# Kernel optimization log

Hardware: AMD Instinct MI355X
Metric: run time of the kernel (lower is better)

Reference implementation:

```python
import jax, jax.numpy as jnp
import numpy as np

GRID_SIZE = 3
SPLINE_ORDER = 3

def make_grid():
    # grid_range=[-1,1], h=2/grid_size; extended grid of length grid_size+2k+1 = 10
    h = 2.0 / GRID_SIZE
    return (jnp.arange(-SPLINE_ORDER, GRID_SIZE + SPLINE_ORDER + 1, dtype=jnp.float32) * h - 1.0)

def b_splines(x, grid):
    # x: [N, F] -> bases [N, F, grid_size+spline_order]
    xg = x[..., None]
    bases = ((xg >= grid[:-1]) & (xg < grid[1:])).astype(x.dtype)
    for j in range(1, SPLINE_ORDER + 1):
        left = (xg - grid[: -(j + 1)]) / (grid[j:-1] - grid[: -(j + 1)])
        right = (grid[j + 1:] - xg) / (grid[j + 1:] - grid[1:-j])
        bases = left * bases[..., :-1] + right * bases[..., 1:]
    return bases

def kan_linear(x, base_w, spline_w, scaler, grid):
    # x: [N, F]; base_w: [O, F]; spline_w: [O, F, G]; scaler: [O, F]
    base = jax.nn.silu(x) @ base_w.T
    sb = b_splines(x, grid)                      # [N, F, G]
    spl = jnp.einsum('nfg,ofg->no', sb, spline_w * scaler[..., None])
    return base + spl

def kan_conv3x3(x, base_w, spline_w, scaler, grid):
    # x: [B, C, H, W]; 3x3 kernel, pad 1, stride 1 -> [B, O, H, W]
    B, C, H, W = x.shape
    patches = jax.lax.conv_general_dilated_patches(
        x, (3, 3), (1, 1), ((1, 1), (1, 1)))     # [B, C*9, H, W]
    p = patches.transpose(0, 2, 3, 1).reshape(B * H * W, C * 9)
    y = kan_linear(p, base_w, spline_w, scaler, grid)
    return y.reshape(B, H, W, -1).transpose(0, 3, 1, 2)

def maxpool2(x):
    return jax.lax.reduce_window(x, -jnp.inf, jax.lax.max,
                                 (1, 1, 2, 2), (1, 1, 2, 2), 'VALID')

def setup_inputs() -> dict:
    key = jax.random.key(0)
    ks = jax.random.split(key, 12)
    s = 0.1
    return {
        'x': jax.random.normal(ks[0], (256, 3, 32, 32), jnp.float32),
        'c1_base_w': jax.random.normal(ks[1], (8, 27), jnp.float32) * s,
        'c1_spline_w': jax.random.normal(ks[2], (8, 27, 6), jnp.float32) * s,
        'c1_scaler': jax.random.normal(ks[3], (8, 27), jnp.float32) * s,
        'c2_base_w': jax.random.normal(ks[4], (16, 72), jnp.float32) * s,
        'c2_spline_w': jax.random.normal(ks[5], (16, 72, 6), jnp.float32) * s,
        'c2_scaler': jax.random.normal(ks[6], (16, 72), jnp.float32) * s,
        'c3_base_w': jax.random.normal(ks[7], (32, 144), jnp.float32) * s,
        'c3_spline_w': jax.random.normal(ks[8], (32, 144, 6), jnp.float32) * s,
        'c3_scaler': jax.random.normal(ks[9], (32, 144), jnp.float32) * s,
        'lin_w': jax.random.normal(ks[10], (100, 512), jnp.float32) * s,
        'lin_b': jax.random.normal(ks[11], (100,), jnp.float32) * s,
    }

def reference(x, c1_base_w, c1_spline_w, c1_scaler,
              c2_base_w, c2_spline_w, c2_scaler,
              c3_base_w, c3_spline_w, c3_scaler,
              lin_w, lin_b):
    grid = make_grid()
    h = maxpool2(kan_conv3x3(x, c1_base_w, c1_spline_w, c1_scaler, grid))   # [B,8,16,16]
    h = maxpool2(kan_conv3x3(h, c2_base_w, c2_spline_w, c2_scaler, grid))   # [B,16,8,8]
    h = maxpool2(kan_conv3x3(h, c3_base_w, c3_spline_w, c3_scaler, grid))   # [B,32,4,4]
    h = h.reshape(h.shape[0], -1)                                           # [B,512]
    return h @ lin_w.T + lin_b                                              # [B,100]
```

## Files before the change

kernel.cpp:

```cpp
#include <hip/hip_runtime.h>
#include <math.h>


#define BATCH 256

typedef short bf16x8 __attribute__((ext_vector_type(8)));
typedef float f32x4  __attribute__((ext_vector_type(4)));

__device__ __forceinline__ unsigned f2bf(float f) {
    unsigned u = __float_as_uint(f);
    u += 0x7fffu + ((u >> 16) & 1u);
    return u >> 16;
}
__device__ __forceinline__ unsigned pk2(float a, float b) {
    return f2bf(a) | (f2bf(b) << 16);
}

__device__ __forceinline__ void bspline_basis(float x, float bs[6]) {
    const float h = 2.0f / 3.0f;
    float g[10];
#pragma unroll
    for (int i = 0; i < 10; ++i) g[i] = (float)(i - 3) * h - 1.0f;
    float b[9];
#pragma unroll
    for (int i = 0; i < 9; ++i) b[i] = (x >= g[i] && x < g[i + 1]) ? 1.0f : 0.0f;
#pragma unroll
    for (int j = 1; j <= 3; ++j) {
        const float inv_d = 1.0f / ((float)j * h);
#pragma unroll
        for (int i = 0; i + j < 9; ++i) {
            float left  = (x - g[i]) * inv_d;
            float right = (g[i + j + 1] - x) * inv_d;
            b[i] = left * b[i] + right * b[i + 1];
        }
    }
#pragma unroll
    for (int i = 0; i < 6; ++i) bs[i] = b[i];
}

__device__ __forceinline__ uint4 act_record(float val) {
    float silu = val / (1.0f + __expf(-val));
    float bs[6];
    bspline_basis(val, bs);
    uint4 r;
    r.x = pk2(silu, bs[0]);
    r.y = pk2(bs[1], bs[2]);
    r.z = pk2(bs[3], bs[4]);
    r.w = f2bf(bs[5]);
    return r;
}

__device__ __forceinline__ uint4 fuse_w(const float* bw, const float* sw,
                                        const float* sc, int j) {
    float s = sc[j];
    uint4 r;
    r.x = pk2(bw[j],             sw[j * 6 + 0] * s);
    r.y = pk2(sw[j * 6 + 1] * s, sw[j * 6 + 2] * s);
    r.z = pk2(sw[j * 6 + 3] * s, sw[j * 6 + 4] * s);
    r.w = f2bf(sw[j * 6 + 5] * s);
    return r;
}

__global__ __launch_bounds__(512, 4) void kan_l1(
        const float* __restrict__ x,
        const float* __restrict__ bw, const float* __restrict__ sw,
        const float* __restrict__ sc,
        const float* __restrict__ bw3, const float* __restrict__ sw3,
        const float* __restrict__ sc3,
        uint4* __restrict__ w3g,
        float* __restrict__ out) {
    constexpr int C = 3, H = 32, W = 32, F = 27, FP = 28, NS = 7;
    constexpr int RT = 18, TC = 34, NT = 512;

    __shared__ uint4 s_act[C * RT * TC];
    __shared__ uint4 s_w[FP * 16];

    const int tid = threadIdx.x;
    const int bid = blockIdx.x;
    const int b   = bid >> 1;
    const int v   = bid & 1;

    if (bid < 9) {
        int i = bid * NT + tid;
        if (i < 4608) {
            int o = i / 144, fp = i % 144;
            w3g[fp * 32 + o] = fuse_w(bw3, sw3, sc3, i);
        }
    }

    for (int i = tid; i < FP * 16; i += NT) {
        int fp = i >> 4, o = i & 15;
        uint4 r = make_uint4(0u, 0u, 0u, 0u);
        if (fp < F && o < 8) r = fuse_w(bw, sw, sc, o * F + fp);
        s_w[i] = r;
    }

    const int r0 = 16 * v - 1;
    const float* xb = x + (size_t)b * C * H * W;
    for (int i = tid; i < C * RT * TC; i += NT) {
        int cc  = i / (RT * TC);
        int rr  = (i / TC) % RT;
        int col = i % TC;
        int gr = r0 + rr, gc = col - 1;
        float val = 0.0f;
        if ((unsigned)gr < (unsigned)H && (unsigned)gc < (unsigned)W)
            val = xb[(cc * H + gr) * W + gc];
        s_act[i] = act_record(val);
    }
    __syncthreads();

    const int lane = tid & 63;
    const int wv   = tid >> 6;
    const int kg   = lane >> 4;
    const int oc   = lane & 15;
    const int m    = lane & 15;

    bf16x8 bfr[NS];
#pragma unroll
    for (int s = 0; s < NS; ++s)
        bfr[s] = *reinterpret_cast<const bf16x8*>(&s_w[(4 * s + kg) * 16 + oc]);

    int pixoff[4];
#pragma unroll
    for (int t = 0; t < 4; ++t)
        pixoff[t] = (2 * wv + (t >> 1)) * TC + 16 * (t & 1) + m;

    f32x4 acc[4];
#pragma unroll
    for (int t = 0; t < 4; ++t) acc[t] = (f32x4){0.f, 0.f, 0.f, 0.f};

#pragma unroll
    for (int s = 0; s < NS; ++s) {
        int tp = 4 * s + kg;
        tp = (tp > F - 1) ? F - 1 : tp;
        int c  = tp / 9;
        int t9 = tp - 9 * c;
        int ky = t9 / 3;
        int kx = t9 - 3 * ky;
        int base = (c * RT + ky) * TC + kx;
#pragma unroll
        for (int t = 0; t < 4; ++t) {
            bf16x8 a = *reinterpret_cast<const bf16x8*>(&s_act[base + pixoff[t]]);
            acc[t] = __builtin_amdgcn_mfma_f32_16x16x32_bf16(a, bfr[s], acc[t], 0, 0, 0);
        }
    }

    if (oc < 8) {
        f32x4 e0, e1;
#pragma unroll
        for (int p = 0; p < 4; ++p) {
            e0[p] = fmaxf(acc[0][p], acc[2][p]);
            e1[p] = fmaxf(acc[1][p], acc[3][p]);
        }
        float* op = out + (((size_t)b * 8 + oc) * 16 + (8 * v + wv)) * 16;
        op[2 * kg]         = fmaxf(e0[0], e0[1]);
        op[2 * kg + 1]     = fmaxf(e0[2], e0[3]);
        op[8 + 2 * kg]     = fmaxf(e1[0], e1[1]);
        op[8 + 2 * kg + 1] = fmaxf(e1[2], e1[3]);
    }
}

__global__ __launch_bounds__(512, 2) void kan_l2l3lin(
        const float* __restrict__ h1,
        const float* __restrict__ bw2, const float* __restrict__ sw2,
        const float* __restrict__ sc2,
        const uint4* __restrict__ w3g,
        const float* __restrict__ lin_w, const float* __restrict__ lin_b,
        float* __restrict__ out) {
    constexpr int NT = 512;
    __shared__ alignas(16) unsigned char s_mem[59904];
    uint4* s_act2 = (uint4*)s_mem;
    uint4* s_w2   = (uint4*)(s_mem + 41472);
    float* s_h2   = (float*)s_mem;
    uint4* s_act3 = (uint4*)(s_mem + 4096);
    float* s_h3   = (float*)s_mem;

    const int tid = threadIdx.x;
    const int n   = blockIdx.x;
    const int lane = tid & 63;
    const int wv   = tid >> 6;
    const int kg   = lane >> 4;
    const int oc   = lane & 15;
    const int m    = lane & 15;

    for (int i = tid; i < 72 * 16; i += NT) {
        int fp = i >> 4, o = i & 15;
        s_w2[i] = fuse_w(bw2, sw2, sc2, o * 72 + fp);
    }
    const float* xb = h1 + (size_t)n * 8 * 16 * 16;
    for (int i = tid; i < 8 * 18 * 18; i += NT) {
        int cc  = i / 324;
        int rr  = (i / 18) % 18;
        int col = i % 18;
        int gr = rr - 1, gc = col - 1;
        float val = 0.0f;
        if ((unsigned)gr < 16u && (unsigned)gc < 16u)
            val = xb[(cc * 16 + gr) * 16 + gc];
        s_act2[i] = act_record(val);
    }
    __syncthreads();

    {
        bf16x8 bfr2[18];
#pragma unroll
        for (int s = 0; s < 18; ++s)
            bfr2[s] = *reinterpret_cast<const bf16x8*>(&s_w2[(4 * s + kg) * 16 + oc]);
        const int p0 = (2 * wv) * 18 + m;
        const int p1 = (2 * wv + 1) * 18 + m;
        f32x4 a0 = (f32x4){0.f, 0.f, 0.f, 0.f};
        f32x4 a1 = (f32x4){0.f, 0.f, 0.f, 0.f};
#pragma unroll
        for (int s = 0; s < 18; ++s) {
            int tp = 4 * s + kg;
            int c  = tp / 9;
            int t9 = tp - 9 * c;
            int ky = t9 / 3;
            int kx = t9 - 3 * ky;
            int base = (c * 18 + ky) * 18 + kx;
            bf16x8 av0 = *reinterpret_cast<const bf16x8*>(&s_act2[base + p0]);
            a0 = __builtin_amdgcn_mfma_f32_16x16x32_bf16(av0, bfr2[s], a0, 0, 0, 0);
            bf16x8 av1 = *reinterpret_cast<const bf16x8*>(&s_act2[base + p1]);
            a1 = __builtin_amdgcn_mfma_f32_16x16x32_bf16(av1, bfr2[s], a1, 0, 0, 0);
        }
        float e0 = fmaxf(a0[0], a1[0]);
        float e1 = fmaxf(a0[1], a1[1]);
        float e2 = fmaxf(a0[2], a1[2]);
        float e3 = fmaxf(a0[3], a1[3]);
        __syncthreads();
        s_h2[(oc * 8 + wv) * 8 + 2 * kg]     = fmaxf(e0, e1);
        s_h2[(oc * 8 + wv) * 8 + 2 * kg + 1] = fmaxf(e2, e3);
    }
    __syncthreads();

    for (int i = tid; i < 16 * 10 * 10; i += NT) {
        int cc  = i / 100;
        int rr  = (i / 10) % 10;
        int col = i % 10;
        int gr = rr - 1, gc = col - 1;
        float val = 0.0f;
        if ((unsigned)gr < 8u && (unsigned)gc < 8u)
            val = s_h2[(cc * 8 + gr) * 8 + gc];
        s_act3[i] = act_record(val);
    }
    __syncthreads();

    {
        const int mt  = wv & 3;
        const int o03 = 16 * (wv >> 2);
        bf16x8 bfr3[36];
#pragma unroll
        for (int s = 0; s < 36; ++s)
            bfr3[s] = *reinterpret_cast<const bf16x8*>(&w3g[(4 * s + kg) * 32 + o03 + oc]);
        const int poff = (2 * mt + (m >> 3)) * 10 + (m & 7);
        f32x4 a3 = (f32x4){0.f, 0.f, 0.f, 0.f};
#pragma unroll
        for (int s = 0; s < 36; ++s) {
            int tp = 4 * s + kg;
            int c  = tp / 9;
            int t9 = tp - 9 * c;
            int ky = t9 / 3;
            int kx = t9 - 3 * ky;
            int base = (c * 10 + ky) * 10 + kx;
            bf16x8 av = *reinterpret_cast<const bf16x8*>(&s_act3[base + poff]);
            a3 = __builtin_amdgcn_mfma_f32_16x16x32_bf16(av, bfr3[s], a3, 0, 0, 0);
        }
        float q0 = fmaxf(a3[0], a3[1]);
        float q1 = fmaxf(a3[2], a3[3]);
        float y0 = fmaxf(q0, __shfl_xor(q0, 32));
        float y1 = fmaxf(q1, __shfl_xor(q1, 32));
        if (kg < 2) {
            s_h3[(o03 + oc) * 16 + mt * 4 + 2 * kg]     = y0;
            s_h3[(o03 + oc) * 16 + mt * 4 + 2 * kg + 1] = y1;
        }
    }
    __syncthreads();

    {
        const float4* hf = (const float4*)s_h3;
        const float4 h0v = hf[lane];
        const float4 h1v = hf[lane + 64];
#pragma unroll 1
        for (int o = wv; o < 100; o += 8) {
            const float4* wr = (const float4*)(lin_w + (size_t)o * 512);
            float4 w0 = wr[lane];
            float4 w1 = wr[lane + 64];
            float p = w0.x * h0v.x + w0.y * h0v.y + w0.z * h0v.z + w0.w * h0v.w
                    + w1.x * h1v.x + w1.y * h1v.y + w1.z * h1v.z + w1.w * h1v.w;
            p += __shfl_xor(p, 32);
            p += __shfl_xor(p, 16);
            p += __shfl_xor(p, 8);
            p += __shfl_xor(p, 4);
            p += __shfl_xor(p, 2);
            p += __shfl_xor(p, 1);
            if (lane == 0) out[(size_t)n * 100 + o] = p + lin_b[o];
        }
    }
}

extern "C" void kernel_launch(void* const* d_in, const int* in_sizes, int n_in,
                              void* d_out, int out_size, void* d_ws, size_t ws_size,
                              hipStream_t stream) {
    const float* x     = (const float*)d_in[0];
    const float* c1_bw = (const float*)d_in[1];
    const float* c1_sw = (const float*)d_in[2];
    const float* c1_sc = (const float*)d_in[3];
    const float* c2_bw = (const float*)d_in[4];
    const float* c2_sw = (const float*)d_in[5];
    const float* c2_sc = (const float*)d_in[6];
    const float* c3_bw = (const float*)d_in[7];
    const float* c3_sw = (const float*)d_in[8];
    const float* c3_sc = (const float*)d_in[9];
    const float* lin_w = (const float*)d_in[10];
    const float* lin_b = (const float*)d_in[11];
    float* out = (float*)d_out;

    float* ws = (float*)d_ws;
    float* h1 = ws;
    uint4* w3g = (uint4*)(h1 + 524288);

    kan_l1<<<512, 512, 0, stream>>>(x, c1_bw, c1_sw, c1_sc,
                                    c3_bw, c3_sw, c3_sc, w3g, h1);
    kan_l2l3lin<<<256, 512, 0, stream>>>(h1, c2_bw, c2_sw, c2_sc,
                                         w3g, lin_w, lin_b, out);
}
```

Measured before the change: 104.8 us.

## Fuse all KAN layers into one kernel with per-sample block and LDS-resident h1

Merges the layer-1 kernel into the layer-2/3/linear kernel so each block processes one sample end to end. The layer-1 output stays in shared memory as bf16 instead of going through global workspace, and layer-3 weights are fused per block into shared memory rather than being precomputed into global memory by a separate kernel. The MFMA chains are split across two accumulators to shorten the dependency chain. The cost is fewer blocks (256 at 512 threads) doing layer 1 serially in two halves, plus redundant per-block weight fusion for layer 3 with extra barriers, which lowers parallelism.

```diff
diff --git a/kernel.cpp b/kernel.cpp
--- a/kernel.cpp
+++ b/kernel.cpp
@@ -11,6 +11,9 @@
     unsigned u = __float_as_uint(f);
     u += 0x7fffu + ((u >> 16) & 1u);
     return u >> 16;
+}
+__device__ __forceinline__ float bf2f(unsigned short u) {
+    return __uint_as_float(((unsigned)u) << 16);
 }
 __device__ __forceinline__ unsigned pk2(float a, float b) {
     return f2bf(a) | (f2bf(b) << 16);
@@ -61,141 +64,111 @@
     return r;
 }
 
-__global__ __launch_bounds__(512, 4) void kan_l1(
+__global__ __launch_bounds__(512, 2) void kan_all(
         const float* __restrict__ x,
-        const float* __restrict__ bw, const float* __restrict__ sw,
-        const float* __restrict__ sc,
-        const float* __restrict__ bw3, const float* __restrict__ sw3,
-        const float* __restrict__ sc3,
-        uint4* __restrict__ w3g,
+        const float* __restrict__ bw1, const float* __restrict__ sw1, const float* __restrict__ sc1,
+        const float* __restrict__ bw2, const float* __restrict__ sw2, const float* __restrict__ sc2,
+        const float* __restrict__ bw3, const float* __restrict__ sw3, const float* __restrict__ sc3,
+        const float* __restrict__ lin_w, const float* __restrict__ lin_b,
         float* __restrict__ out) {
-    constexpr int C = 3, H = 32, W = 32, F = 27, FP = 28, NS = 7;
-    constexpr int RT = 18, TC = 34, NT = 512;
-
-    __shared__ uint4 s_act[C * RT * TC];
-    __shared__ uint4 s_w[FP * 16];
-
-    const int tid = threadIdx.x;
-    const int bid = blockIdx.x;
-    const int b   = bid >> 1;
-    const int v   = bid & 1;
-
-    if (bid < 9) {
-        int i = bid * NT + tid;
-        if (i < 4608) {
-            int o = i / 144, fp = i % 144;
-            w3g[fp * 32 + o] = fuse_w(bw3, sw3, sc3, i);
-        }
-    }
-
-    for (int i = tid; i < FP * 16; i += NT) {
-        int fp = i >> 4, o = i & 15;
-        uint4 r = make_uint4(0u, 0u, 0u, 0u);
-        if (fp < F && o < 8) r = fuse_w(bw, sw, sc, o * F + fp);
-        s_w[i] = r;
-    }
-
-    const int r0 = 16 * v - 1;
-    const float* xb = x + (size_t)b * C * H * W;
-    for (int i = tid; i < C * RT * TC; i += NT) {
-        int cc  = i / (RT * TC);
-        int rr  = (i / TC) % RT;
-        int col = i % TC;
-        int gr = r0 + rr, gc = col - 1;
-        float val = 0.0f;
-        if ((unsigned)gr < (unsigned)H && (unsigned)gc < (unsigned)W)
-            val = xb[(cc * H + gr) * W + gc];
-        s_act[i] = act_record(val);
-    }
-    __syncthreads();
-
+    constexpr int NT = 512;
+    __shared__ alignas(16) unsigned char s_mem[64000];
+    unsigned short* s_h1 = (unsigned short*)s_mem;
+    uint4* s_act1 = (uint4*)(s_mem + 4096);
+    uint4* s_w1   = (uint4*)(s_mem + 33472);
+    uint4* s_act2 = (uint4*)(s_mem + 4096);
+    uint4* s_w2   = (uint4*)(s_mem + 45568);
+    float* s_h2   = (float*)s_mem;
+    uint4* s_w3c  = (uint4*)(s_mem + 4096);
+    uint4* s_act3 = (uint4*)(s_mem + 4096);
+    float* s_h3   = (float*)s_mem;
+
+    const int tid  = threadIdx.x;
+    const int n    = blockIdx.x;
     const int lane = tid & 63;
     const int wv   = tid >> 6;
     const int kg   = lane >> 4;
     const int oc   = lane & 15;
     const int m    = lane & 15;
 
-    bf16x8 bfr[NS];
-#pragma unroll
-    for (int s = 0; s < NS; ++s)
-        bfr[s] = *reinterpret_cast<const bf16x8*>(&s_w[(4 * s + kg) * 16 + oc]);
-
-    int pixoff[4];
-#pragma unroll
-    for (int t = 0; t < 4; ++t)
-        pixoff[t] = (2 * wv + (t >> 1)) * TC + 16 * (t & 1) + m;
-
-    f32x4 acc[4];
-#pragma unroll
-    for (int t = 0; t < 4; ++t) acc[t] = (f32x4){0.f, 0.f, 0.f, 0.f};
-
-#pragma unroll
-    for (int s = 0; s < NS; ++s) {
-        int tp = 4 * s + kg;
-        tp = (tp > F - 1) ? F - 1 : tp;
-        int c  = tp / 9;
-        int t9 = tp - 9 * c;
-        int ky = t9 / 3;
-        int kx = t9 - 3 * ky;
-        int base = (c * RT + ky) * TC + kx;
-#pragma unroll
-        for (int t = 0; t < 4; ++t) {
-            bf16x8 a = *reinterpret_cast<const bf16x8*>(&s_act[base + pixoff[t]]);
-            acc[t] = __builtin_amdgcn_mfma_f32_16x16x32_bf16(a, bfr[s], acc[t], 0, 0, 0);
-        }
-    }
-
-    if (oc < 8) {
-        f32x4 e0, e1;
-#pragma unroll
-        for (int p = 0; p < 4; ++p) {
-            e0[p] = fmaxf(acc[0][p], acc[2][p]);
-            e1[p] = fmaxf(acc[1][p], acc[3][p]);
-        }
-        float* op = out + (((size_t)b * 8 + oc) * 16 + (8 * v + wv)) * 16;
-        op[2 * kg]         = fmaxf(e0[0], e0[1]);
-        op[2 * kg + 1]     = fmaxf(e0[2], e0[3]);
-        op[8 + 2 * kg]     = fmaxf(e1[0], e1[1]);
-        op[8 + 2 * kg + 1] = fmaxf(e1[2], e1[3]);
-    }
-}
-
-__global__ __launch_bounds__(512, 2) void kan_l2l3lin(
-        const float* __restrict__ h1,
-        const float* __restrict__ bw2, const float* __restrict__ sw2,
-        const float* __restrict__ sc2,
-        const uint4* __restrict__ w3g,
-        const float* __restrict__ lin_w, const float* __restrict__ lin_b,
-        float* __restrict__ out) {
-    constexpr int NT = 512;
-    __shared__ alignas(16) unsigned char s_mem[59904];
-    uint4* s_act2 = (uint4*)s_mem;
-    uint4* s_w2   = (uint4*)(s_mem + 41472);
-    float* s_h2   = (float*)s_mem;
-    uint4* s_act3 = (uint4*)(s_mem + 4096);
-    float* s_h3   = (float*)s_mem;
-
-    const int tid = threadIdx.x;
-    const int n   = blockIdx.x;
-    const int lane = tid & 63;
-    const int wv   = tid >> 6;
-    const int kg   = lane >> 4;
-    const int oc   = lane & 15;
-    const int m    = lane & 15;
-
-    for (int i = tid; i < 72 * 16; i += NT) {
+    for (int i = tid; i < 448; i += NT) {
+        int fp = i >> 4, o = i & 15;
+        uint4 r = make_uint4(0u, 0u, 0u, 0u);
+        if (fp < 27 && o < 8) r = fuse_w(bw1, sw1, sc1, o * 27 + fp);
+        s_w1[i] = r;
+    }
+
+    const float* xb = x + (size_t)n * 3 * 32 * 32;
+#pragma unroll 1
+    for (int v = 0; v < 2; ++v) {
+        __syncthreads();
+        const int r0 = 16 * v - 1;
+        for (int i = tid; i < 1836; i += NT) {
+            int cc  = i / 612;
+            int rr  = (i / 34) % 18;
+            int col = i % 34;
+            int gr = r0 + rr, gc = col - 1;
+            float val = 0.0f;
+            if ((unsigned)gr < 32u && (unsigned)gc < 32u)
+                val = xb[(cc * 32 + gr) * 32 + gc];
+            s_act1[i] = act_record(val);
+        }
+        __syncthreads();
+
+        bf16x8 bfr[7];
+#pragma unroll
+        for (int s = 0; s < 7; ++s)
+            bfr[s] = *reinterpret_cast<const bf16x8*>(&s_w1[(4 * s + kg) * 16 + oc]);
+        int pixoff[4];
+#pragma unroll
+        for (int t = 0; t < 4; ++t)
+            pixoff[t] = (2 * wv + (t >> 1)) * 34 + 16 * (t & 1) + m;
+        f32x4 acc[4];
+#pragma unroll
+        for (int t = 0; t < 4; ++t) acc[t] = (f32x4){0.f, 0.f, 0.f, 0.f};
+#pragma unroll
+        for (int s = 0; s < 7; ++s) {
+            int tp = 4 * s + kg;
+            tp = (tp > 26) ? 26 : tp;
+            int c  = tp / 9;
+            int t9 = tp - 9 * c;
+            int ky = t9 / 3;
+            int kx = t9 - 3 * ky;
+            int base = (c * 18 + ky) * 34 + kx;
+#pragma unroll
+            for (int t = 0; t < 4; ++t) {
+                bf16x8 a = *reinterpret_cast<const bf16x8*>(&s_act1[base + pixoff[t]]);
+                acc[t] = __builtin_amdgcn_mfma_f32_16x16x32_bf16(a, bfr[s], acc[t], 0, 0, 0);
+            }
+        }
+        if (oc < 8) {
+            f32x4 e0, e1;
+#pragma unroll
+            for (int p = 0; p < 4; ++p) {
+                e0[p] = fmaxf(acc[0][p], acc[2][p]);
+                e1[p] = fmaxf(acc[1][p], acc[3][p]);
+            }
+            unsigned short* hp = s_h1 + ((oc * 16) + (8 * v + wv)) * 16;
+            hp[2 * kg]         = (unsigned short)f2bf(fmaxf(e0[0], e0[1]));
+            hp[2 * kg + 1]     = (unsigned short)f2bf(fmaxf(e0[2], e0[3]));
+            hp[8 + 2 * kg]     = (unsigned short)f2bf(fmaxf(e1[0], e1[1]));
+            hp[8 + 2 * kg + 1] = (unsigned short)f2bf(fmaxf(e1[2], e1[3]));
+        }
+    }
+    __syncthreads();
+
+    for (int i = tid; i < 1152; i += NT) {
         int fp = i >> 4, o = i & 15;
         s_w2[i] = fuse_w(bw2, sw2, sc2, o * 72 + fp);
     }
-    const float* xb = h1 + (size_t)n * 8 * 16 * 16;
-    for (int i = tid; i < 8 * 18 * 18; i += NT) {
+    for (int i = tid; i < 2592; i += NT) {
         int cc  = i / 324;
         int rr  = (i / 18) % 18;
         int col = i % 18;
         int gr = rr - 1, gc = col - 1;
         float val = 0.0f;
         if ((unsigned)gr < 16u && (unsigned)gc < 16u)
-            val = xb[(cc * 16 + gr) * 16 + gc];
+            val = bf2f(s_h1[(cc * 16 + gr) * 16 + gc]);
         s_act2[i] = act_record(val);
     }
     __syncthreads();
@@ -206,9 +179,8 @@
         for (int s = 0; s < 18; ++s)
             bfr2[s] = *reinterpret_cast<const bf16x8*>(&s_w2[(4 * s + kg) * 16 + oc]);
         const int p0 = (2 * wv) * 18 + m;
-        const int p1 = (2 * wv + 1) * 18 + m;
-        f32x4 a0 = (f32x4){0.f, 0.f, 0.f, 0.f};
-        f32x4 a1 = (f32x4){0.f, 0.f, 0.f, 0.f};
+        const int p1 = p0 + 18;
+        f32x4 a0 = (f32x4){0.f, 0.f, 0.f, 0.f}, a1 = a0, b0 = a0, b1 = a0;
 #pragma unroll
         for (int s = 0; s < 18; ++s) {
             int tp = 4 * s + kg;
@@ -218,21 +190,51 @@
             int kx = t9 - 3 * ky;
             int base = (c * 18 + ky) * 18 + kx;
             bf16x8 av0 = *reinterpret_cast<const bf16x8*>(&s_act2[base + p0]);
-            a0 = __builtin_amdgcn_mfma_f32_16x16x32_bf16(av0, bfr2[s], a0, 0, 0, 0);
             bf16x8 av1 = *reinterpret_cast<const bf16x8*>(&s_act2[base + p1]);
-            a1 = __builtin_amdgcn_mfma_f32_16x16x32_bf16(av1, bfr2[s], a1, 0, 0, 0);
-        }
+            if (s < 9) {
+                a0 = __builtin_amdgcn_mfma_f32_16x16x32_bf16(av0, bfr2[s], a0, 0, 0, 0);
+                a1 = __builtin_amdgcn_mfma_f32_16x16x32_bf16(av1, bfr2[s], a1, 0, 0, 0);
+            } else {
+                b0 = __builtin_amdgcn_mfma_f32_16x16x32_bf16(av0, bfr2[s], b0, 0, 0, 0);
+                b1 = __builtin_amdgcn_mfma_f32_16x16x32_bf16(av1, bfr2[s], b1, 0, 0, 0);
+            }
+        }
+        a0 = a0 + b0;
+        a1 = a1 + b1;
         float e0 = fmaxf(a0[0], a1[0]);
         float e1 = fmaxf(a0[1], a1[1]);
         float e2 = fmaxf(a0[2], a1[2]);
         float e3 = fmaxf(a0[3], a1[3]);
-        __syncthreads();
         s_h2[(oc * 8 + wv) * 8 + 2 * kg]     = fmaxf(e0, e1);
         s_h2[(oc * 8 + wv) * 8 + 2 * kg + 1] = fmaxf(e2, e3);
     }
     __syncthreads();
 
-    for (int i = tid; i < 16 * 10 * 10; i += NT) {
+    bf16x8 bfr3[36];
+    for (int i = tid; i < 2304; i += NT) {
+        int fp = i >> 4, o = i & 15;
+        s_w3c[i] = fuse_w(bw3, sw3, sc3, o * 144 + fp);
+    }
+    __syncthreads();
+    if (wv < 4) {
+#pragma unroll
+        for (int s = 0; s < 36; ++s)
+            bfr3[s] = *reinterpret_cast<const bf16x8*>(&s_w3c[(4 * s + kg) * 16 + oc]);
+    }
+    __syncthreads();
+    for (int i = tid; i < 2304; i += NT) {
+        int fp = i >> 4, o = 16 + (i & 15);
+        s_w3c[i] = fuse_w(bw3, sw3, sc3, o * 144 + fp);
+    }
+    __syncthreads();
+    if (wv >= 4) {
+#pragma unroll
+        for (int s = 0; s < 36; ++s)
+            bfr3[s] = *reinterpret_cast<const bf16x8*>(&s_w3c[(4 * s + kg) * 16 + oc]);
+    }
+    __syncthreads();
+
+    for (int i = tid; i < 1600; i += NT) {
         int cc  = i / 100;
         int rr  = (i / 10) % 10;
         int col = i % 10;
@@ -247,12 +249,8 @@
     {
         const int mt  = wv & 3;
         const int o03 = 16 * (wv >> 2);
-        bf16x8 bfr3[36];
-#pragma unroll
-        for (int s = 0; s < 36; ++s)
-            bfr3[s] = *reinterpret_cast<const bf16x8*>(&w3g[(4 * s + kg) * 32 + o03 + oc]);
         const int poff = (2 * mt + (m >> 3)) * 10 + (m & 7);
-        f32x4 a3 = (f32x4){0.f, 0.f, 0.f, 0.f};
+        f32x4 a3 = (f32x4){0.f, 0.f, 0.f, 0.f}, a3b = a3;
 #pragma unroll
         for (int s = 0; s < 36; ++s) {
             int tp = 4 * s + kg;
@@ -262,8 +260,12 @@
             int kx = t9 - 3 * ky;
             int base = (c * 10 + ky) * 10 + kx;
             bf16x8 av = *reinterpret_cast<const bf16x8*>(&s_act3[base + poff]);
-            a3 = __builtin_amdgcn_mfma_f32_16x16x32_bf16(av, bfr3[s], a3, 0, 0, 0);
-        }
+            if (s < 18)
+                a3 = __builtin_amdgcn_mfma_f32_16x16x32_bf16(av, bfr3[s], a3, 0, 0, 0);
+            else
+                a3b = __builtin_amdgcn_mfma_f32_16x16x32_bf16(av, bfr3[s], a3b, 0, 0, 0);
+        }
+        a3 = a3 + a3b;
         float q0 = fmaxf(a3[0], a3[1]);
         float q1 = fmaxf(a3[2], a3[3]);
         float y0 = fmaxf(q0, __shfl_xor(q0, 32));
@@ -314,12 +316,10 @@
     const float* lin_b = (const float*)d_in[11];
     float* out = (float*)d_out;
 
-    float* ws = (float*)d_ws;
-    float* h1 = ws;
-    uint4* w3g = (uint4*)(h1 + 524288);
-
-    kan_l1<<<512, 512, 0, stream>>>(x, c1_bw, c1_sw, c1_sc,
-                                    c3_bw, c3_sw, c3_sc, w3g, h1);
-    kan_l2l3lin<<<256, 512, 0, stream>>>(h1, c2_bw, c2_sw, c2_sc,
-                                         w3g, lin_w, lin_b, out);
-}
+    kan_all<<<256, 512, 0, stream>>>(
+        x,
+        c1_bw, c1_sw, c1_sc,
+        c2_bw, c2_sw, c2_sc,
+        c3_bw, c3_sw, c3_sc,
+        lin_w, lin_b, out);
+}
```

Measured after the change: 109.5 us. 1.04x slower.
